# Kernel tuning notes

Hardware: AMD Instinct MI355X
Metric: run time of the kernel (lower is better)

The kernel has to match this reference:

```python
import jax, jax.numpy as jnp
import numpy as np
import math

B, S, D, H = 4, 4096, 768, 64

def setup_inputs() -> dict:
    key = jax.random.key(0)
    ks = jax.random.split(key, 4)
    scale = 1.0 / math.sqrt(D)
    return {
        "X": jax.random.normal(ks[0], (B, S, D), dtype=jnp.float32),
        "Wq": jax.random.normal(ks[1], (D, H), dtype=jnp.float32) * scale,
        "bq": jnp.zeros((H,), dtype=jnp.float32),
        "Wk": jax.random.normal(ks[2], (D, H), dtype=jnp.float32) * scale,
        "bk": jnp.zeros((H,), dtype=jnp.float32),
        "Wv": jax.random.normal(ks[3], (D, H), dtype=jnp.float32) * scale,
        "bv": jnp.zeros((H,), dtype=jnp.float32),
    }

def reference(X, Wq, bq, Wk, bk, Wv, bv):
    # Single-head causal scaled-dot-product attention (dropout p=0 / eval mode).
    Q = X @ Wq + bq            # [B, S, H]
    K = X @ Wk + bk            # [B, S, H]
    V = X @ Wv + bv            # [B, S, H]
    head_size = Q.shape[-1]
    scores = jnp.einsum('bqh,bkh->bqk', Q, K) / jnp.sqrt(jnp.asarray(head_size, Q.dtype))
    causal = jnp.tril(jnp.ones((Q.shape[1], Q.shape[1]), dtype=bool))  # [S, S]
    scores = jnp.where(causal[None, :, :], scores, -jnp.inf)
    attn = jax.nn.softmax(scores, axis=-1)   # [B, S, S]
    return jnp.einsum('bqk,bkh->bqh', attn, V)
```

## Files before the change

kernel.cpp:

```cpp
#include <hip/hip_runtime.h>
#include <math.h>

#define BB 4
#define SS 4096
#define DD 768
#define HH 64
#define MM (BB * SS)

typedef __attribute__((ext_vector_type(8))) short bf16x8;
typedef __attribute__((ext_vector_type(4))) float f32x4;

__device__ inline unsigned short f2bf(float f) {
    union { float f; unsigned u; } x; x.f = f;
    unsigned r = x.u + 0x7fffu + ((x.u >> 16) & 1u);
    return (unsigned short)(r >> 16);
}

__device__ inline unsigned cvtpk(float a, float b) {
    unsigned r;
    asm("v_cvt_pk_bf16_f32 %0, %1, %2" : "=v"(r) : "v"(a), "v"(b));
    return r;
}

__device__ inline unsigned short* swzp(unsigned short* base, int byteoff) {
    byteoff ^= ((byteoff >> 7) & 7) << 4;
    return (unsigned short*)((char*)base + byteoff);
}

__global__ __launch_bounds__(256) void wt_kernel(
    const float* __restrict__ Wq, const float* __restrict__ Wk, const float* __restrict__ Wv,
    unsigned short* __restrict__ Wt)
{
    const int kt = blockIdx.x;
    const int sel = blockIdx.y;
    const int k0 = kt * 64;
    const float* W = (sel == 0) ? Wq : (sel == 1) ? Wk : Wv;
    __shared__ float Ws[64][68];
    const int t = threadIdx.x;
    #pragma unroll
    for (int j = 0; j < 4; ++j) {
        const int fl = t + j * 256;
        const int row = fl >> 4, c4 = (fl & 15) * 4;
        float4 v = *reinterpret_cast<const float4*>(&W[(size_t)(k0 + row) * HH + c4]);
        Ws[row][c4 + 0] = v.x; Ws[row][c4 + 1] = v.y;
        Ws[row][c4 + 2] = v.z; Ws[row][c4 + 3] = v.w;
    }
    __syncthreads();
    const int n = t >> 2;
    const int c8 = (t & 3) * 16;
    unsigned short tmp[16];
    #pragma unroll
    for (int j = 0; j < 16; ++j) tmp[j] = f2bf(Ws[c8 + j][n]);
    unsigned short* dst = &Wt[((size_t)sel * 64 + n) * DD + k0 + c8];
    *reinterpret_cast<bf16x8*>(dst)     = *reinterpret_cast<bf16x8*>(&tmp[0]);
    *reinterpret_cast<bf16x8*>(dst + 8) = *reinterpret_cast<bf16x8*>(&tmp[8]);
}

#define VTP 40
__global__ __launch_bounds__(512) void qkv_proj_kernel(
    const float* __restrict__ X, const unsigned short* __restrict__ Wt,
    const float* __restrict__ bq, const float* __restrict__ bk, const float* __restrict__ bv,
    unsigned short* __restrict__ Qb, unsigned short* __restrict__ Kb,
    unsigned short* __restrict__ Vt)
{
    __shared__ unsigned short Alds[32 * 64];
    __shared__ unsigned short Blds[192 * 64];

    const int tid = threadIdx.x;
    const int rowBase = blockIdx.x * 32;
    const int w = tid >> 6;
    const int ms = w & 1;
    const int nq = w >> 1;
    const int lane = tid & 63;
    const int lhi = lane >> 4, llo = lane & 15;

    f32x4 acc[3] = {{0,0,0,0},{0,0,0,0},{0,0,0,0}};

    const int arow = tid >> 4;
    const int ac   = (tid & 15) * 4;

    float4 xA, xB;
    bf16x8 bA[3], bB[3];

    auto loadP = [&](int kb, float4& x0, bf16x8 (&bb)[3]) {
        const int kBase = kb * 64;
        x0 = *reinterpret_cast<const float4*>(&X[(size_t)(rowBase + arow) * DD + kBase + ac]);
        #pragma unroll
        for (int i = 0; i < 3; ++i) {
            const int u = tid + i * 512;
            const int n = u >> 3, c8 = (u & 7) * 8;
            bb[i] = *reinterpret_cast<const bf16x8*>(&Wt[(size_t)n * DD + kBase + c8]);
        }
    };
    auto writeP = [&](const float4& x0, bf16x8 (&bb)[3]) {
        uint2 pk;
        pk.x = cvtpk(x0.x, x0.y);
        pk.y = cvtpk(x0.z, x0.w);
        *reinterpret_cast<uint2*>(swzp(Alds, (arow * 64 + ac) * 2)) = pk;
        #pragma unroll
        for (int i = 0; i < 3; ++i) {
            const int u = tid + i * 512;
            const int n = u >> 3, c8 = (u & 7) * 8;
            *reinterpret_cast<bf16x8*>(swzp(Blds, (n * 64 + c8) * 2)) = bb[i];
        }
    };

    loadP(0, xA, bA);

    for (int kb = 0; kb < DD / 64; ++kb) {
        __syncthreads();
        if ((kb & 1) == 0) {
            writeP(xA, bA);
            if (kb + 1 < DD / 64) loadP(kb + 1, xB, bB);
        } else {
            writeP(xB, bB);
            if (kb + 1 < DD / 64) loadP(kb + 1, xA, bA);
        }
        __syncthreads();

        #pragma unroll
        for (int kk = 0; kk < 2; ++kk) {
            const int aoff = kk * 32 + lhi * 8;
            bf16x8 af = *reinterpret_cast<const bf16x8*>(
                swzp(Alds, ((ms * 16 + llo) * 64 + aoff) * 2));
            #pragma unroll
            for (int nt = 0; nt < 3; ++nt) {
                bf16x8 bf = *reinterpret_cast<const bf16x8*>(
                    swzp(Blds, ((nq * 48 + nt * 16 + llo) * 64 + aoff) * 2));
                acc[nt] = __builtin_amdgcn_mfma_f32_16x16x32_bf16(af, bf, acc[nt], 0, 0, 0);
            }
        }
    }

    __syncthreads();
    unsigned short* VtLds = Blds;

    #pragma unroll
    for (int nt = 0; nt < 3; ++nt) {
        const int n = nq * 48 + nt * 16 + llo;
        const int sel = n >> 6;
        const int nn = n & 63;
        const float bias = (sel == 0) ? bq[nn] : (sel == 1) ? bk[nn] : bv[nn];
        if (sel == 0) {
            #pragma unroll
            for (int r = 0; r < 4; ++r) {
                const int row = rowBase + ms * 16 + lhi * 4 + r;
                Qb[(size_t)row * HH + nn] = f2bf((acc[nt][r] + bias) * 0.125f);
            }
        } else if (sel == 1) {
            #pragma unroll
            for (int r = 0; r < 4; ++r) {
                const int row = rowBase + ms * 16 + lhi * 4 + r;
                Kb[(size_t)row * HH + nn] = f2bf(acc[nt][r] + bias);
            }
        } else {
            uint2 pk;
            pk.x = cvtpk(acc[nt][0] + bias, acc[nt][1] + bias);
            pk.y = cvtpk(acc[nt][2] + bias, acc[nt][3] + bias);
            *reinterpret_cast<uint2*>(&VtLds[nn * VTP + ms * 16 + lhi * 4]) = pk;
        }
    }
    __syncthreads();
    if (tid < 256) {
        const int nn = tid >> 2;
        const int s8 = (tid & 3) * 8;
        const int bb = rowBase >> 12;
        const int sbase = rowBase & (SS - 1);
        bf16x8 v = *reinterpret_cast<const bf16x8*>(&VtLds[nn * VTP + s8]);
        *reinterpret_cast<bf16x8*>(&Vt[((size_t)bb * HH + nn) * SS + sbase + s8]) = v;
    }
}

union SMemA {
    struct {
        unsigned short K[2 * 4096];
        unsigned short V[2 * 4096];
        unsigned short Pl[8][16][72];
    } st;
    struct { float O[4][16][68]; float ml[4][16][2]; } cb;
};

__global__ __launch_bounds__(512, 4) void attn_partial_kernel(
    const unsigned short* __restrict__ Qg, const unsigned short* __restrict__ Kg,
    const unsigned short* __restrict__ Vtg, float* __restrict__ out,
    float* __restrict__ Po, float* __restrict__ Pml)
{
    __shared__ SMemA sm;

    const int idx = blockIdx.x;
    const int l = idx >> 2;
    const int b = idx & 3;
    int qb, c;
    if (l < 49)       { qb = 15 + l;        c = 0; }
    else if (l < 82)  { qb = 31 + (l - 49); c = 1; }
    else if (l < 99)  { qb = 47 + (l - 82); c = 2; }
    else if (l == 99) { qb = 63;            c = 3; }
    else {
        const int j = l - 100;
        const int s = 15 - (j >> 2);
        const int k = j & 3;
        qb = (s - 1) + 16 * k;
        c = k;
    }

    const int tid = threadIdx.x;
    const int q0 = qb * 64;
    const int w   = tid >> 6;
    const int g   = w >> 2;
    const int wq  = w & 3;
    const int lane = tid & 63;
    const int lhi = lane >> 4, llo = lane & 15;
    const int qw0 = q0 + wq * 16;
    const int qme = qw0 + llo;

    const int ntiles = qb + 1;
    const int base0 = c * 16;
    const int endT = min(base0 + 16, ntiles);
    const int nsteps = (endT - base0 + 1) >> 1;
    const int nch = qb / 16 + 1;

    const unsigned short* Kbase = Kg  + (size_t)b * SS * HH;
    const unsigned short* Vbase = Vtg + (size_t)b * HH * SS;

    bf16x8 qf0, qf1;
    {
        const unsigned short* qrow = Qg + ((size_t)b * SS + qme) * HH + lhi * 8;
        qf0 = *reinterpret_cast<const bf16x8*>(qrow);
        qf1 = *reinterpret_cast<const bf16x8*>(qrow + 32);
    }

    float m = -INFINITY, lsum = 0.f;
    f32x4 acc[4] = {{0,0,0,0},{0,0,0,0},{0,0,0,0},{0,0,0,0}};

    const int srow = tid >> 3;
    const int sc8  = (tid & 7) * 8;

    bf16x8 rA[4] = {{0,0,0,0,0,0,0,0},{0,0,0,0,0,0,0,0},{0,0,0,0,0,0,0,0},{0,0,0,0,0,0,0,0}};
    bf16x8 rB[4] = {{0,0,0,0,0,0,0,0},{0,0,0,0,0,0,0,0},{0,0,0,0,0,0,0,0},{0,0,0,0,0,0,0,0}};

    auto load_step = [&](int base, bf16x8 (&rg)[4]) {
        #pragma unroll
        for (int i = 0; i < 4; ++i) {
            const int t = base + (i & 1);
            if (t < endT) {
                rg[i] = (i < 2)
                    ? *reinterpret_cast<const bf16x8*>(&Kbase[(size_t)(t * 64 + srow) * HH + sc8])
                    : *reinterpret_cast<const bf16x8*>(&Vbase[(size_t)srow * SS + t * 64 + sc8]);
            }
        }
    };
    auto write_step = [&](bf16x8 (&rg)[4]) {
        const int ro = (srow * 64 + sc8) * 2;
        *reinterpret_cast<bf16x8*>(swzp(sm.st.K, ro))         = rg[0];
        *reinterpret_cast<bf16x8*>(swzp(sm.st.K, 8192 + ro))  = rg[1];
        *reinterpret_cast<bf16x8*>(swzp(sm.st.V, ro))         = rg[2];
        *reinterpret_cast<bf16x8*>(swzp(sm.st.V, 8192 + ro))  = rg[3];
    };

    load_step(base0, rA);

    for (int stp = 0; stp < nsteps; ++stp) {
        const int base = base0 + stp * 2;
        __syncthreads();
        if ((stp & 1) == 0) {
            write_step(rA);
            if (stp + 1 < nsteps) load_step(base + 2, rB);
        } else {
            write_step(rB);
            if (stp + 1 < nsteps) load_step(base + 2, rA);
        }
        __syncthreads();

        const int lt = base + g;
        if (lt < endT) {
            const int k0 = lt * 64;
            const int tb = g * 8192;

            f32x4 s[4] = {{0,0,0,0},{0,0,0,0},{0,0,0,0},{0,0,0,0}};
            __builtin_amdgcn_s_setprio(1);
            #pragma unroll
            for (int kt = 0; kt < 4; ++kt) {
                const int rbo = tb + ((kt * 16 + llo) * 64) * 2;
                bf16x8 ka = *reinterpret_cast<const bf16x8*>(swzp(sm.st.K, rbo + lhi * 16));
                bf16x8 kb = *reinterpret_cast<const bf16x8*>(swzp(sm.st.K, rbo + 64 + lhi * 16));
                s[kt] = __builtin_amdgcn_mfma_f32_16x16x32_bf16(ka, qf0, s[kt], 0, 0, 0);
                s[kt] = __builtin_amdgcn_mfma_f32_16x16x32_bf16(kb, qf1, s[kt], 0, 0, 0);
            }
            __builtin_amdgcn_s_setprio(0);

            if (k0 + 63 > qw0) {
                #pragma unroll
                for (int kt = 0; kt < 4; ++kt) {
                    #pragma unroll
                    for (int r = 0; r < 4; ++r) {
                        const int key = k0 + kt * 16 + lhi * 4 + r;
                        if (key > qme) s[kt][r] = -INFINITY;
                    }
                }
            }

            float mx = s[0][0];
            #pragma unroll
            for (int kt = 0; kt < 4; ++kt)
                #pragma unroll
                for (int r = 0; r < 4; ++r) mx = fmaxf(mx, s[kt][r]);
            mx = fmaxf(mx, __shfl_xor(mx, 16));
            mx = fmaxf(mx, __shfl_xor(mx, 32));
            if (!__all(mx - m <= 8.0f)) {
                const float mn = fmaxf(m, mx);
                const float corr = __expf(m - mn);
                lsum *= corr;
                #pragma unroll
                for (int dt = 0; dt < 4; ++dt)
                    #pragma unroll
                    for (int r = 0; r < 4; ++r) acc[dt][r] *= corr;
                m = mn;
            }
            float ps = 0.f;
            #pragma unroll
            for (int kt = 0; kt < 4; ++kt)
                #pragma unroll
                for (int r = 0; r < 4; ++r) { s[kt][r] = __expf(s[kt][r] - m); ps += s[kt][r]; }
            ps += __shfl_xor(ps, 16);
            ps += __shfl_xor(ps, 32);
            lsum += ps;

            #pragma unroll
            for (int kt = 0; kt < 4; ++kt) {
                uint2 pk;
                pk.x = cvtpk(s[kt][0], s[kt][1]);
                pk.y = cvtpk(s[kt][2], s[kt][3]);
                *reinterpret_cast<uint2*>(&sm.st.Pl[w][llo][kt * 16 + lhi * 4]) = pk;
            }
            bf16x8 pf0 = *reinterpret_cast<const bf16x8*>(&sm.st.Pl[w][llo][lhi * 8]);
            bf16x8 pf1 = *reinterpret_cast<const bf16x8*>(&sm.st.Pl[w][llo][32 + lhi * 8]);

            __builtin_amdgcn_s_setprio(1);
            #pragma unroll
            for (int dt = 0; dt < 4; ++dt) {
                const int rbo = tb + ((dt * 16 + llo) * 64) * 2;
                bf16x8 va = *reinterpret_cast<const bf16x8*>(swzp(sm.st.V, rbo + lhi * 16));
                bf16x8 vb = *reinterpret_cast<const bf16x8*>(swzp(sm.st.V, rbo + 64 + lhi * 16));
                acc[dt] = __builtin_amdgcn_mfma_f32_16x16x32_bf16(va, pf0, acc[dt], 0, 0, 0);
                acc[dt] = __builtin_amdgcn_mfma_f32_16x16x32_bf16(vb, pf1, acc[dt], 0, 0, 0);
            }
            __builtin_amdgcn_s_setprio(0);
        }
    }

    __syncthreads();
    if (g == 1) {
        #pragma unroll
        for (int dt = 0; dt < 4; ++dt) {
            float4 o4 = {acc[dt][0], acc[dt][1], acc[dt][2], acc[dt][3]};
            *reinterpret_cast<float4*>(&sm.cb.O[wq][llo][dt * 16 + lhi * 4]) = o4;
        }
        if (lhi == 0) { sm.cb.ml[wq][llo][0] = m; sm.cb.ml[wq][llo][1] = lsum; }
    }
    __syncthreads();
    if (g == 0) {
        const float mg = sm.cb.ml[wq][llo][0];
        const float lg = sm.cb.ml[wq][llo][1];
        const float M  = fmaxf(m, mg);
        const float a0 = __expf(m - M);
        const float a1 = __expf(mg - M);
        const float L  = lsum * a0 + lg * a1;
        if (nch == 1) {
            const float invL = 1.f / L;
            float* orow = out + ((size_t)b * SS + qme) * HH;
            #pragma unroll
            for (int dt = 0; dt < 4; ++dt) {
                const float4 o2 = *reinterpret_cast<const float4*>(&sm.cb.O[wq][llo][dt * 16 + lhi * 4]);
                float4 o;
                o.x = (acc[dt][0] * a0 + o2.x * a1) * invL;
                o.y = (acc[dt][1] * a0 + o2.y * a1) * invL;
                o.z = (acc[dt][2] * a0 + o2.z * a1) * invL;
                o.w = (acc[dt][3] * a0 + o2.w * a1) * invL;
                *reinterpret_cast<float4*>(&orow[dt * 16 + lhi * 4]) = o;
            }
        } else {
            float* PoT  = Po  + (((size_t)(b * 64 + qb) * 4 + c) << 12);
            float* PmlT = Pml + (((size_t)(b * 64 + qb) * 4 + c) << 7);
            const int row = wq * 16 + llo;
            #pragma unroll
            for (int dt = 0; dt < 4; ++dt) {
                const float4 o2 = *reinterpret_cast<const float4*>(&sm.cb.O[wq][llo][dt * 16 + lhi * 4]);
                float4 o;
                o.x = acc[dt][0] * a0 + o2.x * a1;
                o.y = acc[dt][1] * a0 + o2.y * a1;
                o.z = acc[dt][2] * a0 + o2.z * a1;
                o.w = acc[dt][3] * a0 + o2.w * a1;
                *reinterpret_cast<float4*>(&PoT[row * 64 + dt * 16 + lhi * 4]) = o;
            }
            if (lhi == 0) { PmlT[row] = M; PmlT[64 + row] = L; }
        }
    }
}

__global__ __launch_bounds__(256) void combine_kernel(
    const float* __restrict__ Po, const float* __restrict__ Pml, float* __restrict__ out)
{
    const int qt = 16 + blockIdx.x;
    const int b  = blockIdx.y;
    const int nch = qt / 16 + 1;
    const int t = threadIdx.x;
    const int row = t >> 2;
    const int col0 = (t & 3) * 16;
    const size_t baseIdx = (size_t)(b * 64 + qt) * 4;

    float mv[4], lv[4], a[4];
    float M = -INFINITY;
    for (int cc = 0; cc < nch; ++cc) {
        const float* PmlT = Pml + ((baseIdx + cc) << 7);
        mv[cc] = PmlT[row];
        lv[cc] = PmlT[64 + row];
        M = fmaxf(M, mv[cc]);
    }
    float L = 0.f;
    for (int cc = 0; cc < nch; ++cc) { a[cc] = __expf(mv[cc] - M); L += a[cc] * lv[cc]; }
    const float invL = 1.f / L;

    #pragma unroll
    for (int j = 0; j < 4; ++j) {
        float4 s = {0.f, 0.f, 0.f, 0.f};
        for (int cc = 0; cc < nch; ++cc) {
            const float4 v = *reinterpret_cast<const float4*>(
                &Po[((baseIdx + cc) << 12) + row * 64 + col0 + j * 4]);
            s.x += a[cc] * v.x; s.y += a[cc] * v.y;
            s.z += a[cc] * v.z; s.w += a[cc] * v.w;
        }
        s.x *= invL; s.y *= invL; s.z *= invL; s.w *= invL;
        *reinterpret_cast<float4*>(&out[((size_t)b * SS + qt * 64 + row) * HH + col0 + j * 4]) = s;
    }
}

extern "C" void kernel_launch(void* const* d_in, const int* in_sizes, int n_in,
                              void* d_out, int out_size, void* d_ws, size_t ws_size,
                              hipStream_t stream)
{
    const float* X  = (const float*)d_in[0];
    const float* Wq = (const float*)d_in[1];
    const float* bq = (const float*)d_in[2];
    const float* Wk = (const float*)d_in[3];
    const float* bk = (const float*)d_in[4];
    const float* Wv = (const float*)d_in[5];
    const float* bv = (const float*)d_in[6];

    unsigned short* Qb = (unsigned short*)d_ws;
    unsigned short* Kb = Qb + (size_t)MM * HH;
    unsigned short* Vt = Kb + (size_t)MM * HH;
    unsigned short* Wt = Vt + (size_t)MM * HH;
    float* Po  = (float*)(Wt + (size_t)192 * DD);
    float* Pml = Po + ((size_t)BB * 64 * 4 << 12);

    dim3 gw(DD / 64, 3);
    wt_kernel<<<gw, 256, 0, stream>>>(Wq, Wk, Wv, Wt);

    qkv_proj_kernel<<<MM / 32, 512, 0, stream>>>(X, Wt, bq, bk, bv, Qb, Kb, Vt);

    attn_partial_kernel<<<160 * BB, 512, 0, stream>>>(Qb, Kb, Vt, (float*)d_out, Po, Pml);
    dim3 gc(48, BB);
    combine_kernel<<<gc, 256, 0, stream>>>(Po, Pml, (float*)d_out);
}
```

Before: 56.50 us.

## Give each attention wave two 16-row query strips to reuse K/V fragments

The attention block shrinks from 8 to 4 waves, and each wave now processes 32 query rows (two 16-row strips) instead of 16. Each K and V fragment read from LDS feeds twice as many MFMAs, which halves the LDS read traffic per flop, and each thread loads twice as many K/V staging vectors. In exchange, register pressure rises (two sets of accumulators, scores and Q fragments), there are fewer waves per block, and the occupancy hint drops to 3 blocks, which may reduce latency hiding.

```diff
diff --git a/kernel.cpp b/kernel.cpp
--- a/kernel.cpp
+++ b/kernel.cpp
@@ -175,12 +175,12 @@
     struct {
         unsigned short K[2 * 4096];
         unsigned short V[2 * 4096];
-        unsigned short Pl[8][16][72];
+        unsigned short Pl[4][32][72];
     } st;
-    struct { float O[4][16][68]; float ml[4][16][2]; } cb;
+    struct { float O[64][68]; float ml[64][2]; } cb;
 };
 
-__global__ __launch_bounds__(512, 4) void attn_partial_kernel(
+__global__ __launch_bounds__(256, 3) void attn_partial_kernel(
     const unsigned short* __restrict__ Qg, const unsigned short* __restrict__ Kg,
     const unsigned short* __restrict__ Vtg, float* __restrict__ out,
     float* __restrict__ Po, float* __restrict__ Pml)
@@ -205,13 +205,15 @@
 
     const int tid = threadIdx.x;
     const int q0 = qb * 64;
-    const int w   = tid >> 6;
-    const int g   = w >> 2;
-    const int wq  = w & 3;
+    const int w    = tid >> 6;
+    const int g    = w >> 1;
+    const int wq2  = w & 1;
     const int lane = tid & 63;
     const int lhi = lane >> 4, llo = lane & 15;
-    const int qw0 = q0 + wq * 16;
-    const int qme = qw0 + llo;
+    const int qw0A = q0 + wq2 * 32;
+    const int qw0B = qw0A + 16;
+    const int qmeA = qw0A + llo;
+    const int qmeB = qw0B + llo;
 
     const int ntiles = qb + 1;
     const int base0 = c * 16;
@@ -222,39 +224,49 @@
     const unsigned short* Kbase = Kg  + (size_t)b * SS * HH;
     const unsigned short* Vbase = Vtg + (size_t)b * HH * SS;
 
-    bf16x8 qf0, qf1;
+    bf16x8 qfA0, qfA1, qfB0, qfB1;
     {
-        const unsigned short* qrow = Qg + ((size_t)b * SS + qme) * HH + lhi * 8;
-        qf0 = *reinterpret_cast<const bf16x8*>(qrow);
-        qf1 = *reinterpret_cast<const bf16x8*>(qrow + 32);
-    }
-
-    float m = -INFINITY, lsum = 0.f;
-    f32x4 acc[4] = {{0,0,0,0},{0,0,0,0},{0,0,0,0},{0,0,0,0}};
-
-    const int srow = tid >> 3;
-    const int sc8  = (tid & 7) * 8;
-
-    bf16x8 rA[4] = {{0,0,0,0,0,0,0,0},{0,0,0,0,0,0,0,0},{0,0,0,0,0,0,0,0},{0,0,0,0,0,0,0,0}};
-    bf16x8 rB[4] = {{0,0,0,0,0,0,0,0},{0,0,0,0,0,0,0,0},{0,0,0,0,0,0,0,0},{0,0,0,0,0,0,0,0}};
-
-    auto load_step = [&](int base, bf16x8 (&rg)[4]) {
-        #pragma unroll
-        for (int i = 0; i < 4; ++i) {
-            const int t = base + (i & 1);
+        const unsigned short* qa = Qg + ((size_t)b * SS + qmeA) * HH + lhi * 8;
+        qfA0 = *reinterpret_cast<const bf16x8*>(qa);
+        qfA1 = *reinterpret_cast<const bf16x8*>(qa + 32);
+        const unsigned short* qbp = Qg + ((size_t)b * SS + qmeB) * HH + lhi * 8;
+        qfB0 = *reinterpret_cast<const bf16x8*>(qbp);
+        qfB1 = *reinterpret_cast<const bf16x8*>(qbp + 32);
+    }
+
+    float mA = -INFINITY, lsumA = 0.f;
+    float mB = -INFINITY, lsumB = 0.f;
+    f32x4 accA[4] = {{0,0,0,0},{0,0,0,0},{0,0,0,0},{0,0,0,0}};
+    f32x4 accB[4] = {{0,0,0,0},{0,0,0,0},{0,0,0,0},{0,0,0,0}};
+
+    bf16x8 rA[8], rB[8];
+    #pragma unroll
+    for (int i = 0; i < 8; ++i) { rA[i] = bf16x8{0,0,0,0,0,0,0,0}; rB[i] = bf16x8{0,0,0,0,0,0,0,0}; }
+
+    auto load_step = [&](int base, bf16x8 (&rg)[8]) {
+        #pragma unroll
+        for (int i = 0; i < 8; ++i) {
+            const int pt = (i >> 1) & 1;
+            const int t = base + pt;
+            const int u = tid + (i & 1) * 256;
+            const int row = u >> 3, c8 = (u & 7) * 8;
             if (t < endT) {
-                rg[i] = (i < 2)
-                    ? *reinterpret_cast<const bf16x8*>(&Kbase[(size_t)(t * 64 + srow) * HH + sc8])
-                    : *reinterpret_cast<const bf16x8*>(&Vbase[(size_t)srow * SS + t * 64 + sc8]);
+                rg[i] = (i < 4)
+                    ? *reinterpret_cast<const bf16x8*>(&Kbase[(size_t)(t * 64 + row) * HH + c8])
+                    : *reinterpret_cast<const bf16x8*>(&Vbase[(size_t)row * SS + t * 64 + c8]);
             }
         }
     };
-    auto write_step = [&](bf16x8 (&rg)[4]) {
-        const int ro = (srow * 64 + sc8) * 2;
-        *reinterpret_cast<bf16x8*>(swzp(sm.st.K, ro))         = rg[0];
-        *reinterpret_cast<bf16x8*>(swzp(sm.st.K, 8192 + ro))  = rg[1];
-        *reinterpret_cast<bf16x8*>(swzp(sm.st.V, ro))         = rg[2];
-        *reinterpret_cast<bf16x8*>(swzp(sm.st.V, 8192 + ro))  = rg[3];
+    auto write_step = [&](bf16x8 (&rg)[8]) {
+        #pragma unroll
+        for (int i = 0; i < 8; ++i) {
+            const int pt = (i >> 1) & 1;
+            const int u = tid + (i & 1) * 256;
+            const int row = u >> 3, c8 = (u & 7) * 8;
+            const int ro = pt * 8192 + (row * 64 + c8) * 2;
+            if (i < 4) *reinterpret_cast<bf16x8*>(swzp(sm.st.K, ro)) = rg[i];
+            else       *reinterpret_cast<bf16x8*>(swzp(sm.st.V, ro)) = rg[i];
+        }
     };
 
     load_step(base0, rA);
@@ -276,64 +288,91 @@
             const int k0 = lt * 64;
             const int tb = g * 8192;
 
-            f32x4 s[4] = {{0,0,0,0},{0,0,0,0},{0,0,0,0},{0,0,0,0}};
+            f32x4 sA[4] = {{0,0,0,0},{0,0,0,0},{0,0,0,0},{0,0,0,0}};
+            f32x4 sB[4] = {{0,0,0,0},{0,0,0,0},{0,0,0,0},{0,0,0,0}};
             __builtin_amdgcn_s_setprio(1);
             #pragma unroll
             for (int kt = 0; kt < 4; ++kt) {
                 const int rbo = tb + ((kt * 16 + llo) * 64) * 2;
                 bf16x8 ka = *reinterpret_cast<const bf16x8*>(swzp(sm.st.K, rbo + lhi * 16));
                 bf16x8 kb = *reinterpret_cast<const bf16x8*>(swzp(sm.st.K, rbo + 64 + lhi * 16));
-                s[kt] = __builtin_amdgcn_mfma_f32_16x16x32_bf16(ka, qf0, s[kt], 0, 0, 0);
-                s[kt] = __builtin_amdgcn_mfma_f32_16x16x32_bf16(kb, qf1, s[kt], 0, 0, 0);
+                sA[kt] = __builtin_amdgcn_mfma_f32_16x16x32_bf16(ka, qfA0, sA[kt], 0, 0, 0);
+                sA[kt] = __builtin_amdgcn_mfma_f32_16x16x32_bf16(kb, qfA1, sA[kt], 0, 0, 0);
+                sB[kt] = __builtin_amdgcn_mfma_f32_16x16x32_bf16(ka, qfB0, sB[kt], 0, 0, 0);
+                sB[kt] = __builtin_amdgcn_mfma_f32_16x16x32_bf16(kb, qfB1, sB[kt], 0, 0, 0);
             }
             __builtin_amdgcn_s_setprio(0);
 
-            if (k0 + 63 > qw0) {
+            if (k0 + 63 > qw0A) {
                 #pragma unroll
                 for (int kt = 0; kt < 4; ++kt) {
                     #pragma unroll
                     for (int r = 0; r < 4; ++r) {
                         const int key = k0 + kt * 16 + lhi * 4 + r;
-                        if (key > qme) s[kt][r] = -INFINITY;
+                        if (key > qmeA) sA[kt][r] = -INFINITY;
+                        if (key > qmeB) sB[kt][r] = -INFINITY;
                     }
                 }
             }
 
-            float mx = s[0][0];
+            float mxA = sA[0][0], mxB = sB[0][0];
             #pragma unroll
             for (int kt = 0; kt < 4; ++kt)
                 #pragma unroll
-                for (int r = 0; r < 4; ++r) mx = fmaxf(mx, s[kt][r]);
-            mx = fmaxf(mx, __shfl_xor(mx, 16));
-            mx = fmaxf(mx, __shfl_xor(mx, 32));
-            if (!__all(mx - m <= 8.0f)) {
-                const float mn = fmaxf(m, mx);
-                const float corr = __expf(m - mn);
-                lsum *= corr;
+                for (int r = 0; r < 4; ++r) { mxA = fmaxf(mxA, sA[kt][r]); mxB = fmaxf(mxB, sB[kt][r]); }
+            mxA = fmaxf(mxA, __shfl_xor(mxA, 16));
+            mxA = fmaxf(mxA, __shfl_xor(mxA, 32));
+            mxB = fmaxf(mxB, __shfl_xor(mxB, 16));
+            mxB = fmaxf(mxB, __shfl_xor(mxB, 32));
+            if (!__all(mxA - mA <= 8.0f)) {
+                const float mn = fmaxf(mA, mxA);
+                const float corr = __expf(mA - mn);
+                lsumA *= corr;
                 #pragma unroll
                 for (int dt = 0; dt < 4; ++dt)
                     #pragma unroll
-                    for (int r = 0; r < 4; ++r) acc[dt][r] *= corr;
-                m = mn;
-            }
-            float ps = 0.f;
+                    for (int r = 0; r < 4; ++r) accA[dt][r] *= corr;
+                mA = mn;
+            }
+            if (!__all(mxB - mB <= 8.0f)) {
+                const float mn = fmaxf(mB, mxB);
+                const float corr = __expf(mB - mn);
+                lsumB *= corr;
+                #pragma unroll
+                for (int dt = 0; dt < 4; ++dt)
+                    #pragma unroll
+                    for (int r = 0; r < 4; ++r) accB[dt][r] *= corr;
+                mB = mn;
+            }
+            float psA = 0.f, psB = 0.f;
             #pragma unroll
             for (int kt = 0; kt < 4; ++kt)
                 #pragma unroll
-                for (int r = 0; r < 4; ++r) { s[kt][r] = __expf(s[kt][r] - m); ps += s[kt][r]; }
-            ps += __shfl_xor(ps, 16);
-            ps += __shfl_xor(ps, 32);
-            lsum += ps;
+                for (int r = 0; r < 4; ++r) {
+                    sA[kt][r] = __expf(sA[kt][r] - mA); psA += sA[kt][r];
+                    sB[kt][r] = __expf(sB[kt][r] - mB); psB += sB[kt][r];
+                }
+            psA += __shfl_xor(psA, 16);
+            psA += __shfl_xor(psA, 32);
+            psB += __shfl_xor(psB, 16);
+            psB += __shfl_xor(psB, 32);
+            lsumA += psA;
+            lsumB += psB;
 
             #pragma unroll
             for (int kt = 0; kt < 4; ++kt) {
-                uint2 pk;
-                pk.x = cvtpk(s[kt][0], s[kt][1]);
-                pk.y = cvtpk(s[kt][2], s[kt][3]);
-                *reinterpret_cast<uint2*>(&sm.st.Pl[w][llo][kt * 16 + lhi * 4]) = pk;
-            }
-            bf16x8 pf0 = *reinterpret_cast<const bf16x8*>(&sm.st.Pl[w][llo][lhi * 8]);
-            bf16x8 pf1 = *reinterpret_cast<const bf16x8*>(&sm.st.Pl[w][llo][32 + lhi * 8]);
+                uint2 pkA, pkB;
+                pkA.x = cvtpk(sA[kt][0], sA[kt][1]);
+                pkA.y = cvtpk(sA[kt][2], sA[kt][3]);
+                pkB.x = cvtpk(sB[kt][0], sB[kt][1]);
+                pkB.y = cvtpk(sB[kt][2], sB[kt][3]);
+                *reinterpret_cast<uint2*>(&sm.st.Pl[w][llo][kt * 16 + lhi * 4]) = pkA;
+                *reinterpret_cast<uint2*>(&sm.st.Pl[w][16 + llo][kt * 16 + lhi * 4]) = pkB;
+            }
+            bf16x8 pfA0 = *reinterpret_cast<const bf16x8*>(&sm.st.Pl[w][llo][lhi * 8]);
+            bf16x8 pfA1 = *reinterpret_cast<const bf16x8*>(&sm.st.Pl[w][llo][32 + lhi * 8]);
+            bf16x8 pfB0 = *reinterpret_cast<const bf16x8*>(&sm.st.Pl[w][16 + llo][lhi * 8]);
+            bf16x8 pfB1 = *reinterpret_cast<const bf16x8*>(&sm.st.Pl[w][16 + llo][32 + lhi * 8]);
 
             __builtin_amdgcn_s_setprio(1);
             #pragma unroll
@@ -341,58 +380,73 @@
                 const int rbo = tb + ((dt * 16 + llo) * 64) * 2;
                 bf16x8 va = *reinterpret_cast<const bf16x8*>(swzp(sm.st.V, rbo + lhi * 16));
                 bf16x8 vb = *reinterpret_cast<const bf16x8*>(swzp(sm.st.V, rbo + 64 + lhi * 16));
-                acc[dt] = __builtin_amdgcn_mfma_f32_16x16x32_bf16(va, pf0, acc[dt], 0, 0, 0);
-                acc[dt] = __builtin_amdgcn_mfma_f32_16x16x32_bf16(vb, pf1, acc[dt], 0, 0, 0);
+                accA[dt] = __builtin_amdgcn_mfma_f32_16x16x32_bf16(va, pfA0, accA[dt], 0, 0, 0);
+                accA[dt] = __builtin_amdgcn_mfma_f32_16x16x32_bf16(vb, pfA1, accA[dt], 0, 0, 0);
+                accB[dt] = __builtin_amdgcn_mfma_f32_16x16x32_bf16(va, pfB0, accB[dt], 0, 0, 0);
+                accB[dt] = __builtin_amdgcn_mfma_f32_16x16x32_bf16(vb, pfB1, accB[dt], 0, 0, 0);
             }
             __builtin_amdgcn_s_setprio(0);
         }
     }
 
     __syncthreads();
+    const int rowA = wq2 * 32 + llo;
+    const int rowB = rowA + 16;
     if (g == 1) {
         #pragma unroll
         for (int dt = 0; dt < 4; ++dt) {
-            float4 o4 = {acc[dt][0], acc[dt][1], acc[dt][2], acc[dt][3]};
-            *reinterpret_cast<float4*>(&sm.cb.O[wq][llo][dt * 16 + lhi * 4]) = o4;
-        }
-        if (lhi == 0) { sm.cb.ml[wq][llo][0] = m; sm.cb.ml[wq][llo][1] = lsum; }
+            float4 oA = {accA[dt][0], accA[dt][1], accA[dt][2], accA[dt][3]};
+            float4 oB = {accB[dt][0], accB[dt][1], accB[dt][2], accB[dt][3]};
+            *reinterpret_cast<float4*>(&sm.cb.O[rowA][dt * 16 + lhi * 4]) = oA;
+            *reinterpret_cast<float4*>(&sm.cb.O[rowB][dt * 16 + lhi * 4]) = oB;
+        }
+        if (lhi == 0) {
+            sm.cb.ml[rowA][0] = mA; sm.cb.ml[rowA][1] = lsumA;
+            sm.cb.ml[rowB][0] = mB; sm.cb.ml[rowB][1] = lsumB;
+        }
     }
     __syncthreads();
     if (g == 0) {
-        const float mg = sm.cb.ml[wq][llo][0];
-        const float lg = sm.cb.ml[wq][llo][1];
-        const float M  = fmaxf(m, mg);
-        const float a0 = __expf(m - M);
-        const float a1 = __expf(mg - M);
-        const float L  = lsum * a0 + lg * a1;
-        if (nch == 1) {
-            const float invL = 1.f / L;
-            float* orow = out + ((size_t)b * SS + qme) * HH;
-            #pragma unroll
-            for (int dt = 0; dt < 4; ++dt) {
-                const float4 o2 = *reinterpret_cast<const float4*>(&sm.cb.O[wq][llo][dt * 16 + lhi * 4]);
-                float4 o;
-                o.x = (acc[dt][0] * a0 + o2.x * a1) * invL;
-                o.y = (acc[dt][1] * a0 + o2.y * a1) * invL;
-                o.z = (acc[dt][2] * a0 + o2.z * a1) * invL;
-                o.w = (acc[dt][3] * a0 + o2.w * a1) * invL;
-                *reinterpret_cast<float4*>(&orow[dt * 16 + lhi * 4]) = o;
-            }
-        } else {
-            float* PoT  = Po  + (((size_t)(b * 64 + qb) * 4 + c) << 12);
-            float* PmlT = Pml + (((size_t)(b * 64 + qb) * 4 + c) << 7);
-            const int row = wq * 16 + llo;
-            #pragma unroll
-            for (int dt = 0; dt < 4; ++dt) {
-                const float4 o2 = *reinterpret_cast<const float4*>(&sm.cb.O[wq][llo][dt * 16 + lhi * 4]);
-                float4 o;
-                o.x = acc[dt][0] * a0 + o2.x * a1;
-                o.y = acc[dt][1] * a0 + o2.y * a1;
-                o.z = acc[dt][2] * a0 + o2.z * a1;
-                o.w = acc[dt][3] * a0 + o2.w * a1;
-                *reinterpret_cast<float4*>(&PoT[row * 64 + dt * 16 + lhi * 4]) = o;
-            }
-            if (lhi == 0) { PmlT[row] = M; PmlT[64 + row] = L; }
+        #pragma unroll
+        for (int st = 0; st < 2; ++st) {
+            const int row = (st == 0) ? rowA : rowB;
+            const float mreg = (st == 0) ? mA : mB;
+            const float lreg = (st == 0) ? lsumA : lsumB;
+            const f32x4* accp = (st == 0) ? accA : accB;
+            const float mg = sm.cb.ml[row][0];
+            const float lg = sm.cb.ml[row][1];
+            const float M  = fmaxf(mreg, mg);
+            const float a0 = __expf(mreg - M);
+            const float a1 = __expf(mg - M);
+            const float L  = lreg * a0 + lg * a1;
+            if (nch == 1) {
+                const float invL = 1.f / L;
+                float* orow = out + ((size_t)b * SS + q0 + row) * HH;
+                #pragma unroll
+                for (int dt = 0; dt < 4; ++dt) {
+                    const float4 o2 = *reinterpret_cast<const float4*>(&sm.cb.O[row][dt * 16 + lhi * 4]);
+                    float4 o;
+                    o.x = (accp[dt][0] * a0 + o2.x * a1) * invL;
+                    o.y = (accp[dt][1] * a0 + o2.y * a1) * invL;
+                    o.z = (accp[dt][2] * a0 + o2.z * a1) * invL;
+                    o.w = (accp[dt][3] * a0 + o2.w * a1) * invL;
+                    *reinterpret_cast<float4*>(&orow[dt * 16 + lhi * 4]) = o;
+                }
+            } else {
+                float* PoT  = Po  + (((size_t)(b * 64 + qb) * 4 + c) << 12);
+                float* PmlT = Pml + (((size_t)(b * 64 + qb) * 4 + c) << 7);
+                #pragma unroll
+                for (int dt = 0; dt < 4; ++dt) {
+                    const float4 o2 = *reinterpret_cast<const float4*>(&sm.cb.O[row][dt * 16 + lhi * 4]);
+                    float4 o;
+                    o.x = accp[dt][0] * a0 + o2.x * a1;
+                    o.y = accp[dt][1] * a0 + o2.y * a1;
+                    o.z = accp[dt][2] * a0 + o2.z * a1;
+                    o.w = accp[dt][3] * a0 + o2.w * a1;
+                    *reinterpret_cast<float4*>(&PoT[row * 64 + dt * 16 + lhi * 4]) = o;
+                }
+                if (lhi == 0) { PmlT[row] = M; PmlT[64 + row] = L; }
+            }
         }
     }
 }
@@ -458,7 +512,7 @@
 
     qkv_proj_kernel<<<MM / 32, 512, 0, stream>>>(X, Wt, bq, bk, bv, Qb, Kb, Vt);
 
-    attn_partial_kernel<<<160 * BB, 512, 0, stream>>>(Qb, Kb, Vt, (float*)d_out, Po, Pml);
+    attn_partial_kernel<<<160 * BB, 256, 0, stream>>>(Qb, Kb, Vt, (float*)d_out, Po, Pml);
     dim3 gc(48, BB);
     combine_kernel<<<gc, 256, 0, stream>>>(Po, Pml, (float*)d_out);
 }
```

Measured after the change: 65.52 us. +16.0%, slower.
